# Kernel optimization log

Hardware: AMD Instinct MI355X
Metric: run time of the kernel (lower is better)

Reference implementation:

```python
import jax, jax.numpy as jnp
import numpy as np

CAPACITY_FACTOR = 0.5
AUX_LOSS_WEIGHT = 0.01


def setup_inputs() -> dict:
    key = jax.random.key(0)
    k1, k2 = jax.random.split(key)
    B, S, D = 4, 8192, 2048
    hidden = jax.random.normal(k1, (B, S, D), dtype=jnp.float32)
    # glorot-uniform for a (D,) -> scalar projection: limit = sqrt(6/(D+1))
    limit = float(np.sqrt(6.0 / (D + 1)))
    router_weight = jax.random.uniform(k2, (D,), dtype=jnp.float32, minval=-limit, maxval=limit)
    router_bias = jnp.zeros((), dtype=jnp.float32)
    return {"hidden": hidden, "router_weight": router_weight, "router_bias": router_bias}


def reference(hidden, router_weight, router_bias):
    # hidden: [B, S, D] -> per-token scalar logit via matvec
    B, S, D = hidden.shape
    logits = jnp.einsum("bsd,d->bs", hidden, router_weight) + router_bias  # [B, S]
    router_probs = jax.nn.sigmoid(logits)  # [B, S]

    # capacity: top-k tokens per sequence
    k = int(CAPACITY_FACTOR * S)
    _, topk_idx = jax.lax.top_k(router_probs, k)  # [B, k]
    selected_mask = jnp.zeros((B, S), dtype=hidden.dtype).at[
        jnp.arange(B)[:, None], topk_idx
    ].set(1.0)  # [B, S] binary

    # load-balancing aux loss: penalize deviation of mean routing prob
    # from the capacity budget, per batch element
    mean_prob = jnp.mean(router_probs, axis=-1)  # [B]
    auxiliary_loss = AUX_LOSS_WEIGHT * jnp.square(mean_prob - CAPACITY_FACTOR)  # [B]

    return router_probs, selected_mask, auxiliary_loss
```

## Files before the change

kernel.cpp:

```cpp
#include <hip/hip_runtime.h>
#include <math.h>

#define NB 4
#define NS 8192
#define ND 2048
#define NK 4096

__global__ void __launch_bounds__(256)
router_matvec(const float* __restrict__ hidden,
              const float* __restrict__ w,
              const float* __restrict__ bias,
              float* __restrict__ probs)
{
    const int token = blockIdx.x;
    const float* hp = hidden + (size_t)token * ND;
    const int t = threadIdx.x;

    float acc = 0.0f;
#pragma unroll
    for (int j = 0; j < 2; ++j) {
        const int idx = (j * 256 + t) * 4;
        const float4 h  = *reinterpret_cast<const float4*>(hp + idx);
        const float4 ww = *reinterpret_cast<const float4*>(w + idx);
        acc += h.x * ww.x + h.y * ww.y + h.z * ww.z + h.w * ww.w;
    }

#pragma unroll
    for (int off = 32; off; off >>= 1) acc += __shfl_down(acc, off, 64);

    __shared__ float lds[4];
    const int wid = t >> 6, lane = t & 63;
    if (lane == 0) lds[wid] = acc;
    __syncthreads();
    if (t == 0) {
        const float logit = lds[0] + lds[1] + lds[2] + lds[3] + bias[0];
        probs[token] = 1.0f / (1.0f + expf(-logit));
    }
}


__device__ __forceinline__ int block_reduce_int(int v, int* lds)
{
#pragma unroll
    for (int off = 32; off; off >>= 1) v += __shfl_down(v, off, 64);
    const int wid = threadIdx.x >> 6, lane = threadIdx.x & 63;
    __syncthreads();
    if (lane == 0) lds[wid] = v;
    __syncthreads();
    int s = 0;
#pragma unroll
    for (int i = 0; i < 16; ++i) s += lds[i];
    return s;
}

__device__ __forceinline__ float block_reduce_float(float v, float* lds)
{
#pragma unroll
    for (int off = 32; off; off >>= 1) v += __shfl_down(v, off, 64);
    const int wid = threadIdx.x >> 6, lane = threadIdx.x & 63;
    __syncthreads();
    if (lane == 0) lds[wid] = v;
    __syncthreads();
    float s = 0.0f;
#pragma unroll
    for (int i = 0; i < 16; ++i) s += lds[i];
    return s;
}

__global__ void __launch_bounds__(1024)
topk_mask(const float* __restrict__ probs,
          float* __restrict__ mask,
          float* __restrict__ aux)
{
    const int b = blockIdx.x;
    const float* row = probs + b * NS;
    float*      mrow = mask  + b * NS;

    const int t = threadIdx.x;
    const int base = t * 8;
    const int wid = t >> 6, lane = t & 63;

    __shared__ int   ilds[16];
    __shared__ float flds[16];

    float    v[8];
    unsigned u[8];
#pragma unroll
    for (int i = 0; i < 8; ++i) {
        v[i] = row[base + i];
        u[i] = __float_as_uint(v[i]);
    }

    float s = 0.0f;
#pragma unroll
    for (int i = 0; i < 8; ++i) s += v[i];
    const float rowsum = block_reduce_float(s, flds);

    unsigned prefix = 0;
    int kk = NK;
#pragma unroll
    for (int bit = 31; bit >= 0; --bit) {
        const unsigned cand = prefix | (1u << bit);
        const unsigned hm   = ~((1u << bit) - 1u);
        int c = 0;
#pragma unroll
        for (int i = 0; i < 8; ++i) c += ((u[i] & hm) == cand) ? 1 : 0;
        const int tot = block_reduce_int(c, ilds);
        if (tot >= kk) prefix = cand;
        else           kk -= tot;
    }
    const unsigned thr = prefix;
    const int need_ties = kk;

    int eqc = 0;
#pragma unroll
    for (int i = 0; i < 8; ++i) eqc += (u[i] == thr) ? 1 : 0;

    int inc = eqc;
#pragma unroll
    for (int off = 1; off < 64; off <<= 1) {
        const int y = __shfl_up(inc, off, 64);
        if (lane >= off) inc += y;
    }
    __syncthreads();
    if (lane == 63) ilds[wid] = inc;
    __syncthreads();
    if (t == 0) {
        int run = 0;
#pragma unroll
        for (int wv = 0; wv < 16; ++wv) { const int x = ilds[wv]; ilds[wv] = run; run += x; }
    }
    __syncthreads();
    int run = (inc - eqc) + ilds[wid];

#pragma unroll
    for (int i = 0; i < 8; ++i) {
        float m;
        if (u[i] > thr)       m = 1.0f;
        else if (u[i] == thr) { m = (run < need_ties) ? 1.0f : 0.0f; ++run; }
        else                  m = 0.0f;
        mrow[base + i] = m;
    }

    if (t == 0) {
        const float mean = rowsum * (1.0f / (float)NS);
        const float d = mean - 0.5f;
        aux[b] = 0.01f * d * d;
    }
}

extern "C" void kernel_launch(void* const* d_in, const int* in_sizes, int n_in,
                              void* d_out, int out_size, void* d_ws, size_t ws_size,
                              hipStream_t stream)
{
    const float* hidden = (const float*)d_in[0];
    const float* w      = (const float*)d_in[1];
    const float* bias   = (const float*)d_in[2];

    float* out   = (float*)d_out;
    float* probs = out;
    float* mask  = out + NB * NS;
    float* aux   = out + 2 * NB * NS;

    router_matvec<<<NB * NS, 256, 0, stream>>>(hidden, w, bias, probs);
    topk_mask<<<NB, 1024, 0, stream>>>(probs, mask, aux);
}
```

Measured before the change: 67.43 us.

## Assign tokens per wavefront in router matvec with register-cached weights

The router matvec now launches a fixed grid of 2048 blocks in which each wavefront handles several tokens, instead of one 256-thread block per token. The router weights are loaded into registers once per wave and reused across tokens. Hidden-state loads use nontemporal hints, and the reduction is done entirely with wave shuffles, with no LDS or __syncthreads. This aims to remove per-block launch and synchronisation overhead and repeated weight loads. The cost is higher register use per thread and fewer waves in flight to hide memory latency.

```diff
diff --git a/kernel.cpp b/kernel.cpp
--- a/kernel.cpp
+++ b/kernel.cpp
@@ -6,35 +6,50 @@
 #define ND 2048
 #define NK 4096
 
-__global__ void __launch_bounds__(256)
+#define MV_BLOCKS   2048
+#define MV_THREADS  256
+#define MV_WAVES    (MV_BLOCKS * MV_THREADS / 64)
+#define TOK_PER_WAVE ((NB * NS) / MV_WAVES)
+
+typedef float f32x4 __attribute__((ext_vector_type(4)));
+
+__global__ void __launch_bounds__(MV_THREADS)
 router_matvec(const float* __restrict__ hidden,
               const float* __restrict__ w,
               const float* __restrict__ bias,
               float* __restrict__ probs)
 {
-    const int token = blockIdx.x;
-    const float* hp = hidden + (size_t)token * ND;
-    const int t = threadIdx.x;
+    const int t    = threadIdx.x;
+    const int wid  = t >> 6;
+    const int lane = t & 63;
+    const int wave = blockIdx.x * (MV_THREADS / 64) + wid;
 
-    float acc = 0.0f;
+    f32x4 wreg[8];
 #pragma unroll
-    for (int j = 0; j < 2; ++j) {
-        const int idx = (j * 256 + t) * 4;
-        const float4 h  = *reinterpret_cast<const float4*>(hp + idx);
-        const float4 ww = *reinterpret_cast<const float4*>(w + idx);
-        acc += h.x * ww.x + h.y * ww.y + h.z * ww.z + h.w * ww.w;
-    }
+    for (int j = 0; j < 8; ++j)
+        wreg[j] = *reinterpret_cast<const f32x4*>(w + (j * 64 + lane) * 4);
+
+    const float b0 = bias[0];
 
 #pragma unroll
-    for (int off = 32; off; off >>= 1) acc += __shfl_down(acc, off, 64);
+    for (int it = 0; it < TOK_PER_WAVE; ++it) {
+        const int token = wave + it * MV_WAVES;
+        const float* hp = hidden + (size_t)token * ND;
 
-    __shared__ float lds[4];
-    const int wid = t >> 6, lane = t & 63;
-    if (lane == 0) lds[wid] = acc;
-    __syncthreads();
-    if (t == 0) {
-        const float logit = lds[0] + lds[1] + lds[2] + lds[3] + bias[0];
-        probs[token] = 1.0f / (1.0f + expf(-logit));
+        float acc = 0.0f;
+#pragma unroll
+        for (int j = 0; j < 8; ++j) {
+            const f32x4 h = __builtin_nontemporal_load(
+                reinterpret_cast<const f32x4*>(hp + (j * 64 + lane) * 4));
+            acc += h.x * wreg[j].x + h.y * wreg[j].y
+                 + h.z * wreg[j].z + h.w * wreg[j].w;
+        }
+
+#pragma unroll
+        for (int off = 32; off; off >>= 1) acc += __shfl_down(acc, off, 64);
+
+        if (lane == 0)
+            probs[token] = 1.0f / (1.0f + expf(-(acc + b0)));
     }
 }
 
@@ -162,6 +177,6 @@
     float* mask  = out + NB * NS;
     float* aux   = out + 2 * NB * NS;
 
-    router_matvec<<<NB * NS, 256, 0, stream>>>(hidden, w, bias, probs);
+    router_matvec<<<MV_BLOCKS, MV_THREADS, 0, stream>>>(hidden, w, bias, probs);
     topk_mask<<<NB, 1024, 0, stream>>>(probs, mask, aux);
 }
```

New measurement: 72.85 us. 8.0% more time.
